# Kernel tuning notes

Measured on AMD Instinct MI355X. Metric: run time of the kernel, lower is better.

Reference implementation:

```python
import jax, jax.numpy as jnp
import numpy as np

IN_DIM = 256
QK_DIM = IN_DIM // 8


def setup_inputs() -> dict:
    key = jax.random.key(0)
    ks = jax.random.split(key, 6)
    x = jax.random.normal(ks[0], (8, IN_DIM, 64, 64), dtype=jnp.float32)
    # 1x1 conv == per-pixel linear; store weights as [out, in]
    q_w = jax.random.normal(ks[1], (QK_DIM, IN_DIM), dtype=jnp.float32) * (1.0 / np.sqrt(IN_DIM))
    q_b = jax.random.normal(ks[2], (QK_DIM,), dtype=jnp.float32) * 0.01
    v_w = jax.random.normal(ks[3], (IN_DIM, IN_DIM), dtype=jnp.float32) * (1.0 / np.sqrt(IN_DIM))
    v_b = jax.random.normal(ks[4], (IN_DIM,), dtype=jnp.float32) * 0.01
    gamma = jnp.zeros((1,), dtype=jnp.float32) + 0.5  # nonzero so attention branch contributes
    return {"x": x, "q_w": q_w, "q_b": q_b, "v_w": v_w, "v_b": v_b, "gamma": gamma}


def reference(x, q_w, q_b, v_w, v_b, gamma):
    b, c, h, w = x.shape
    n = h * w
    xf = x.reshape(b, c, n)                                    # [b, c, n]
    # NOTE: original forward uses q_conv for BOTH q and k (k_conv unused)
    q = jnp.einsum('oc,bcn->bon', q_w, xf) + q_b[None, :, None]  # [b, d, n]
    proj_q = jnp.transpose(q, (0, 2, 1))                       # [b, n, d]
    energy = jnp.einsum('bid,bdj->bij', proj_q, q)             # [b, n, n]
    attention = jax.nn.softmax(energy, axis=-1)
    v = jnp.einsum('oc,bcn->bon', v_w, xf) + v_b[None, :, None]  # [b, c, n]
    # out[b,c,i] = sum_j v[b,c,j] * attention[b,i,j]
    out = jnp.einsum('bcj,bij->bci', v, attention)
    out = out.reshape(b, c, h, w)
    return gamma * out + x
```

## Files before the change

### kernel.cpp

```cpp
#include <hip/hip_runtime.h>

#define B_   8
#define C_   256
#define D_   32
#define N_   4096
#define FMX  64.0f
#define PSWZ(u) ((u) ^ (((u) >> 3) & 7))
#define VP   4112
#define VBUF 32896

typedef __attribute__((ext_vector_type(8))) short bf8_t;
typedef __attribute__((ext_vector_type(4))) float f4_t;

__device__ __forceinline__ unsigned short f2bf(float f) {
    unsigned int u = __builtin_bit_cast(unsigned int, f);
    u += 0x7FFFu + ((u >> 16) & 1u);
    return (unsigned short)(u >> 16);
}
__device__ __forceinline__ float bf2f(unsigned short h) {
    unsigned int u = ((unsigned int)h) << 16;
    return __builtin_bit_cast(float, u);
}
__device__ __forceinline__ uint4 pack8(const unsigned short* h) {
    uint4 u;
    u.x = h[0] | ((unsigned)h[1] << 16); u.y = h[2] | ((unsigned)h[3] << 16);
    u.z = h[4] | ((unsigned)h[5] << 16); u.w = h[6] | ((unsigned)h[7] << 16);
    return u;
}
__device__ __forceinline__ void gload_lds16(const void* g, void* l) {
    __builtin_amdgcn_global_load_lds(
        (const __attribute__((address_space(1))) unsigned int*)g,
        (__attribute__((address_space(3))) unsigned int*)l, 16, 0, 0);
}

__global__ __launch_bounds__(256) void wprep_kernel(
    const float* __restrict__ qw, const float* __restrict__ vw,
    unsigned short* __restrict__ wqFh, unsigned short* __restrict__ wqFl,
    unsigned short* __restrict__ wvF)
{
    const int tid = blockIdx.x * 256 + threadIdx.x;
    if (tid < 8192) {
        const int k = tid;
        const int rowblk = k >> 9, kk = (k >> 6) & 7, lane = k & 63;
        const int oc = rowblk * 16 + (lane & 15), c0 = kk * 32 + (lane >> 4) * 8;
        const float* src = vw + oc * 256 + c0;
        unsigned short h[8];
        #pragma unroll
        for (int e = 0; e < 8; ++e) h[e] = f2bf(src[e]);
        *(uint4*)(wvF + (size_t)k * 8) = pack8(h);
    } else if (tid < 9216) {
        const int k = tid - 8192;
        const int rowblk = k >> 9, kk = (k >> 6) & 7, lane = k & 63;
        const int oc = rowblk * 16 + (lane & 15), c0 = kk * 32 + (lane >> 4) * 8;
        const float* src = qw + oc * 256 + c0;
        unsigned short h[8], l[8];
        #pragma unroll
        for (int e = 0; e < 8; ++e) {
            h[e] = f2bf(src[e]);
            l[e] = f2bf(src[e] - bf2f(h[e]));
        }
        *(uint4*)(wqFh + (size_t)k * 8) = pack8(h);
        *(uint4*)(wqFl + (size_t)k * 8) = pack8(l);
    }
}

__global__ __launch_bounds__(256, 2) void proj_kernel(
    const float* __restrict__ x, const unsigned short* __restrict__ wqFh,
    const unsigned short* __restrict__ wqFl, const unsigned short* __restrict__ wvF,
    const float* __restrict__ qb, const float* __restrict__ vb,
    unsigned short* __restrict__ qh, unsigned short* __restrict__ ql,
    unsigned short* __restrict__ vF)
{
    __shared__ __align__(16) unsigned short S[18432];

    const int t    = threadIdx.x;
    const int lane = t & 63;
    const int w    = t >> 6;
    const int q4   = lane >> 4;
    const int l15  = lane & 15;
    const int b    = blockIdx.x & 7;
    const int tile = blockIdx.x >> 3;
    const int i0   = tile * 64;

    const float* xb = x + (size_t)b * C_ * N_ + i0 + lane;
    #pragma unroll
    for (int cc = 0; cc < 8; ++cc) {
        const int chi = w * 8 + cc;
        float v[8];
        #pragma unroll
        for (int e = 0; e < 8; ++e) v[e] = xb[(size_t)(chi * 8 + e) * N_];
        unsigned short h[8];
        #pragma unroll
        for (int e = 0; e < 8; ++e) h[e] = f2bf(v[e]);
        *(uint4*)&S[(chi * 64 + lane) * 8] = pack8(h);
    }
    __syncthreads();

    f4_t acc[4][4];
    #pragma unroll
    for (int mt = 0; mt < 4; ++mt)
        #pragma unroll
        for (int nt = 0; nt < 4; ++nt) acc[mt][nt] = (f4_t)0.0f;
    f4_t qacc[2];
    qacc[0] = (f4_t)0.0f; qacc[1] = (f4_t)0.0f;

    #pragma unroll
    for (int kk = 0; kk < 8; ++kk) {
        bf8_t Bh[4];
        #pragma unroll
        for (int nt = 0; nt < 4; ++nt)
            Bh[nt] = *(const bf8_t*)&S[((kk * 4 + q4) * 64 + nt * 16 + l15) * 8];
        bf8_t Av[4];
        #pragma unroll
        for (int mt = 0; mt < 4; ++mt)
            Av[mt] = *(const bf8_t*)&wvF[(size_t)(((w * 4 + mt) * 8 + kk) * 64 + lane) * 8];
        bf8_t Aqh[2], Aql[2];
        #pragma unroll
        for (int mq = 0; mq < 2; ++mq) {
            Aqh[mq] = *(const bf8_t*)&wqFh[(size_t)((mq * 8 + kk) * 64 + lane) * 8];
            Aql[mq] = *(const bf8_t*)&wqFl[(size_t)((mq * 8 + kk) * 64 + lane) * 8];
        }

        #pragma unroll
        for (int mt = 0; mt < 4; ++mt)
            #pragma unroll
            for (int nt = 0; nt < 4; ++nt)
                acc[mt][nt] = __builtin_amdgcn_mfma_f32_16x16x32_bf16(
                    Av[mt], Bh[nt], acc[mt][nt], 0, 0, 0);
        #pragma unroll
        for (int mq = 0; mq < 2; ++mq) {
            qacc[mq] = __builtin_amdgcn_mfma_f32_16x16x32_bf16(Aqh[mq], Bh[w], qacc[mq], 0, 0, 0);
            qacc[mq] = __builtin_amdgcn_mfma_f32_16x16x32_bf16(Aql[mq], Bh[w], qacc[mq], 0, 0, 0);
        }
    }

    {
        const int iq = i0 + w * 16 + l15;
        #pragma unroll
        for (int mq = 0; mq < 2; ++mq) {
            float4 qb4 = *(const float4*)(qb + mq * 16 + q4 * 4);
            float qv[4] = {qacc[mq][0] + qb4.x, qacc[mq][1] + qb4.y,
                           qacc[mq][2] + qb4.z, qacc[mq][3] + qb4.w};
            unsigned short hr[4], lr[4];
            #pragma unroll
            for (int r = 0; r < 4; ++r) {
                hr[r] = f2bf(qv[r]);
                lr[r] = f2bf(qv[r] - bf2f(hr[r]));
            }
            uint2 uh, ul;
            uh.x = hr[0] | ((unsigned)hr[1] << 16); uh.y = hr[2] | ((unsigned)hr[3] << 16);
            ul.x = lr[0] | ((unsigned)lr[1] << 16); ul.y = lr[2] | ((unsigned)lr[3] << 16);
            size_t qoff = ((size_t)b * N_ + iq) * D_ + mq * 16 + q4 * 4;
            *(uint2*)(qh + qoff) = uh;
            *(uint2*)(ql + qoff) = ul;
        }
    }

    __syncthreads();
    #pragma unroll
    for (int mt = 0; mt < 4; ++mt) {
        float4 vb4 = *(const float4*)(vb + w * 64 + mt * 16 + q4 * 4);
        float bias[4] = {vb4.x, vb4.y, vb4.z, vb4.w};
        #pragma unroll
        for (int nt = 0; nt < 4; ++nt)
            #pragma unroll
            for (int r = 0; r < 4; ++r)
                S[(w * 64 + mt * 16 + q4 * 4 + r) * 72 + nt * 16 + l15] =
                    f2bf(acc[mt][nt][r] + bias[r]);
    }
    __syncthreads();
    #pragma unroll
    for (int k2 = 0; k2 < 8; ++k2) {
        uint4 dat = *(const uint4*)&S[t * 72 + k2 * 8];
        *(uint4*)(vF + ((((size_t)b * 64 + tile) * 8 + k2) * 256 + t) * 8) = dat;
    }
}

__global__ __launch_bounds__(256, 2) void attn_kernel(
    const unsigned short* __restrict__ qh, const unsigned short* __restrict__ ql,
    const unsigned short* __restrict__ vF, const float* __restrict__ x,
    const float* __restrict__ gamma_p, float* __restrict__ out)
{
    __shared__ __align__(16) unsigned char SMEM[2 * VBUF];
    __shared__ __align__(16) unsigned short Pb[4096];
    __shared__ __align__(16) float rowl[64];
    float* T = (float*)SMEM;

    const int t    = threadIdx.x;
    const int lane = t & 63;
    const int w    = t >> 6;
    const int q4   = lane >> 4;
    const int l15  = lane & 15;
    const int b    = blockIdx.x & 7;
    const int i0   = (blockIdx.x >> 3) * 64;

    const unsigned short* qhb = qh + (size_t)b * N_ * D_;
    const unsigned short* qlb = ql + (size_t)b * N_ * D_;
    const unsigned short* vFb = vF + (size_t)b * 1048576;

    bf8_t Ah[4], Al[4];
    #pragma unroll
    for (int mt = 0; mt < 4; ++mt) {
        size_t off = (size_t)(i0 + mt * 16 + l15) * D_ + q4 * 8;
        Ah[mt] = *(const bf8_t*)(qhb + off);
        Al[mt] = *(const bf8_t*)(qlb + off);
    }

    auto STAGE = [&](int jt, int buf) {
        const unsigned short* vj = vFb + (size_t)jt * 16384;
        #pragma unroll
        for (int i = 0; i < 8; ++i) {
            const int c = i * 4 + w;
            const int p = c >> 2, sub = c & 3;
            gload_lds16(vj + c * 512 + lane * 8,
                        &SMEM[buf * VBUF + p * VP + sub * 1024]);
        }
    };

    f4_t acc[4][4];
    #pragma unroll
    for (int mt = 0; mt < 4; ++mt)
        #pragma unroll
        for (int nt = 0; nt < 4; ++nt) acc[mt][nt] = (f4_t)0.0f;

    f4_t lacc[4];
    #pragma unroll
    for (int mt = 0; mt < 4; ++mt) lacc[mt] = (f4_t)0.0f;
    bf8_t onesb;
    #pragma unroll
    for (int e = 0; e < 8; ++e) onesb[e] = (short)0x3F80;

    const int jl = w * 16 + l15;
    const int pprt = jl >> 3, jlo = jl & 7;

    size_t koff0 = (size_t)(0 + w * 16 + l15) * D_ + q4 * 8;
    bf8_t Bh = *(const bf8_t*)(qhb + koff0);
    bf8_t Bl = *(const bf8_t*)(qlb + koff0);
    STAGE(0, 0);

    for (int jt = 0; jt < N_ / 64; ++jt) {
        const int cur = jt & 1;

        f4_t s[4];
        #pragma unroll
        for (int mt = 0; mt < 4; ++mt) {
            f4_t a = (f4_t)0.0f;
            a = __builtin_amdgcn_mfma_f32_16x16x32_bf16(Ah[mt], Bh, a, 0, 0, 0);
            a = __builtin_amdgcn_mfma_f32_16x16x32_bf16(Ah[mt], Bl, a, 0, 0, 0);
            a = __builtin_amdgcn_mfma_f32_16x16x32_bf16(Al[mt], Bh, a, 0, 0, 0);
            s[mt] = a;
        }

        unsigned short pu[4][4];
        #pragma unroll
        for (int mt = 0; mt < 4; ++mt)
            #pragma unroll
            for (int r = 0; r < 4; ++r)
                pu[mt][r] = f2bf(__expf(s[mt][r] - FMX));

        __syncthreads();

        #pragma unroll
        for (int mt = 0; mt < 4; ++mt)
            #pragma unroll
            for (int r = 0; r < 4; ++r) {
                int u = pprt * 64 + mt * 16 + q4 * 4 + r;
                Pb[PSWZ(u) * 8 + jlo] = pu[mt][r];
            }

        __syncthreads();

        const int jn = (jt + 1 < N_ / 64) ? jt + 1 : jt;
        size_t koffn = (size_t)(jn * 64 + w * 16 + l15) * D_ + q4 * 8;
        bf8_t Bh_n = *(const bf8_t*)(qhb + koffn);
        bf8_t Bl_n = *(const bf8_t*)(qlb + koffn);
        if (jt + 1 < N_ / 64) STAGE(jt + 1, cur ^ 1);

        #pragma unroll
        for (int kk = 0; kk < 2; ++kk) {
            bf8_t Af[4], Bf[4];
            #pragma unroll
            for (int nt = 0; nt < 4; ++nt)
                Bf[nt] = *(const bf8_t*)&SMEM[cur * VBUF + (kk * 4 + q4) * VP +
                                              (w * 64 + nt * 16 + l15) * 16];
            #pragma unroll
            for (int mt = 0; mt < 4; ++mt) {
                int u = (kk * 4 + q4) * 64 + mt * 16 + l15;
                Af[mt] = *(const bf8_t*)&Pb[PSWZ(u) * 8];
            }
            #pragma unroll
            for (int mt = 0; mt < 4; ++mt)
                #pragma unroll
                for (int nt = 0; nt < 4; ++nt)
                    acc[mt][nt] = __builtin_amdgcn_mfma_f32_16x16x32_bf16(
                        Af[mt], Bf[nt], acc[mt][nt], 0, 0, 0);
            if (w == 3) {
                #pragma unroll
                for (int mt = 0; mt < 4; ++mt)
                    lacc[mt] = __builtin_amdgcn_mfma_f32_16x16x32_bf16(
                        Af[mt], onesb, lacc[mt], 0, 0, 0);
            }
        }

        Bh = Bh_n; Bl = Bl_n;
    }

    __syncthreads();
    if (w == 3 && l15 == 0) {
        #pragma unroll
        for (int mt = 0; mt < 4; ++mt)
            #pragma unroll
            for (int r = 0; r < 4; ++r)
                rowl[mt * 16 + q4 * 4 + r] = lacc[mt][r];
    }
    __syncthreads();

    const float g = gamma_p[0];
    for (int mt = 0; mt < 4; ++mt) {
        float4 rl = *(float4*)(&rowl[mt * 16 + q4 * 4]);
        float inv[4] = { g / rl.x, g / rl.y, g / rl.z, g / rl.w };
        #pragma unroll
        for (int nt = 0; nt < 4; ++nt)
            #pragma unroll
            for (int r = 0; r < 4; ++r)
                T[(w * 64 + nt * 16 + l15) * 17 + q4 * 4 + r] = acc[mt][nt][r] * inv[r];
        __syncthreads();
        #pragma unroll
        for (int pass = 0; pass < 4; ++pass) {
            int c  = pass * 64 + (t >> 2);
            int ii = (t & 3) * 4;
            float4 o;
            o.x = T[c * 17 + ii];     o.y = T[c * 17 + ii + 1];
            o.z = T[c * 17 + ii + 2]; o.w = T[c * 17 + ii + 3];
            size_t goff = ((size_t)b * C_ + c) * N_ + i0 + mt * 16 + ii;
            float4 xv = *(const float4*)(x + goff);
            o.x += xv.x; o.y += xv.y; o.z += xv.z; o.w += xv.w;
            *(float4*)(out + goff) = o;
        }
        __syncthreads();
    }
}

extern "C" void kernel_launch(void* const* d_in, const int* in_sizes, int n_in,
                              void* d_out, int out_size, void* d_ws, size_t ws_size,
                              hipStream_t stream)
{
    const float* x     = (const float*)d_in[0];
    const float* q_w   = (const float*)d_in[1];
    const float* q_b   = (const float*)d_in[2];
    const float* v_w   = (const float*)d_in[3];
    const float* v_b   = (const float*)d_in[4];
    const float* gamma = (const float*)d_in[5];
    float* out = (float*)d_out;

    unsigned short* ws16 = (unsigned short*)d_ws;
    unsigned short* qhp  = ws16;
    unsigned short* qlp  = ws16 + 1048576;
    unsigned short* vFp  = ws16 + 2097152;
    unsigned short* wvF  = ws16 + 10485760;
    unsigned short* wqFh = wvF + 65536;
    unsigned short* wqFl = wqFh + 8192;

    wprep_kernel<<<36, 256, 0, stream>>>(q_w, v_w, wqFh, wqFl, wvF);
    proj_kernel<<<B_ * (N_ / 64), 256, 0, stream>>>(x, wqFh, wqFl, wvF, q_b, v_b,
                                                    qhp, qlp, vFp);
    attn_kernel<<<B_ * (N_ / 64), 256, 0, stream>>>(qhp, qlp, vFp, x, gamma, out);
}
```

Measured before the change: 227.9 us.

## Shrink projection tiles, XOR-swizzle V layout, double-buffer P, and raise MFMA priority

The projection kernel now processes 32-pixel tiles with half the LDS, twice as many blocks and a higher occupancy bound. Its q projection is limited to two waves, and V is written in an XOR-swizzled layout. The attention kernel drops the padded V stride in favour of that swizzle and double-buffers the P tile, which removes one barrier per iteration. It also sets a higher wave priority around the MFMA loop. The aim is better proj occupancy, fewer bank conflicts and fewer syncs, at the cost of more smaller proj blocks and a more complex, coupled layout.

Result: no change. 225.9 us (-0.9%).

```diff
diff --git a/kernel.cpp b/kernel.cpp
--- a/kernel.cpp
+++ b/kernel.cpp
@@ -6,8 +6,7 @@
 #define N_   4096
 #define FMX  64.0f
 #define PSWZ(u) ((u) ^ (((u) >> 3) & 7))
-#define VP   4112
-#define VBUF 32896
+#define VBUF 32768
 
 typedef __attribute__((ext_vector_type(8))) short bf8_t;
 typedef __attribute__((ext_vector_type(4))) float f4_t;
@@ -64,14 +63,14 @@
     }
 }
 
-__global__ __launch_bounds__(256, 2) void proj_kernel(
+__global__ __launch_bounds__(256, 4) void proj_kernel(
     const float* __restrict__ x, const unsigned short* __restrict__ wqFh,
     const unsigned short* __restrict__ wqFl, const unsigned short* __restrict__ wvF,
     const float* __restrict__ qb, const float* __restrict__ vb,
     unsigned short* __restrict__ qh, unsigned short* __restrict__ ql,
     unsigned short* __restrict__ vF)
 {
-    __shared__ __align__(16) unsigned short S[18432];
+    __shared__ __align__(16) unsigned short S[10240];
 
     const int t    = threadIdx.x;
     const int lane = t & 63;
@@ -79,62 +78,65 @@
     const int q4   = lane >> 4;
     const int l15  = lane & 15;
     const int b    = blockIdx.x & 7;
-    const int tile = blockIdx.x >> 3;
-    const int i0   = tile * 64;
-
-    const float* xb = x + (size_t)b * C_ * N_ + i0 + lane;
-    #pragma unroll
-    for (int cc = 0; cc < 8; ++cc) {
-        const int chi = w * 8 + cc;
-        float v[8];
-        #pragma unroll
-        for (int e = 0; e < 8; ++e) v[e] = xb[(size_t)(chi * 8 + e) * N_];
-        unsigned short h[8];
-        #pragma unroll
-        for (int e = 0; e < 8; ++e) h[e] = f2bf(v[e]);
-        *(uint4*)&S[(chi * 64 + lane) * 8] = pack8(h);
-    }
-    __syncthreads();
-
-    f4_t acc[4][4];
+    const int tt   = blockIdx.x >> 3;
+    const int i0   = tt * 32;
+
+    {
+        const int n  = lane & 31;
+        const int hi = lane >> 5;
+        const float* xb = x + (size_t)b * C_ * N_ + i0 + n;
+        #pragma unroll
+        for (int cc = 0; cc < 4; ++cc) {
+            const int chi = w * 8 + cc * 2 + hi;
+            float v[8];
+            #pragma unroll
+            for (int e = 0; e < 8; ++e) v[e] = xb[(size_t)(chi * 8 + e) * N_];
+            unsigned short h[8];
+            #pragma unroll
+            for (int e = 0; e < 8; ++e) h[e] = f2bf(v[e]);
+            *(uint4*)&S[(chi * 32 + (n ^ (chi & 3))) * 8] = pack8(h);
+        }
+    }
+    __syncthreads();
+
+    f4_t acc[4][2];
     #pragma unroll
     for (int mt = 0; mt < 4; ++mt)
         #pragma unroll
-        for (int nt = 0; nt < 4; ++nt) acc[mt][nt] = (f4_t)0.0f;
+        for (int nt = 0; nt < 2; ++nt) acc[mt][nt] = (f4_t)0.0f;
     f4_t qacc[2];
     qacc[0] = (f4_t)0.0f; qacc[1] = (f4_t)0.0f;
 
     #pragma unroll
     for (int kk = 0; kk < 8; ++kk) {
-        bf8_t Bh[4];
-        #pragma unroll
-        for (int nt = 0; nt < 4; ++nt)
-            Bh[nt] = *(const bf8_t*)&S[((kk * 4 + q4) * 64 + nt * 16 + l15) * 8];
+        bf8_t Bh[2];
+        #pragma unroll
+        for (int nt = 0; nt < 2; ++nt)
+            Bh[nt] = *(const bf8_t*)&S[((kk * 4 + q4) * 32 + nt * 16 + (l15 ^ q4)) * 8];
         bf8_t Av[4];
         #pragma unroll
         for (int mt = 0; mt < 4; ++mt)
             Av[mt] = *(const bf8_t*)&wvF[(size_t)(((w * 4 + mt) * 8 + kk) * 64 + lane) * 8];
-        bf8_t Aqh[2], Aql[2];
-        #pragma unroll
-        for (int mq = 0; mq < 2; ++mq) {
-            Aqh[mq] = *(const bf8_t*)&wqFh[(size_t)((mq * 8 + kk) * 64 + lane) * 8];
-            Aql[mq] = *(const bf8_t*)&wqFl[(size_t)((mq * 8 + kk) * 64 + lane) * 8];
-        }
-
-        #pragma unroll
-        for (int mt = 0; mt < 4; ++mt)
-            #pragma unroll
-            for (int nt = 0; nt < 4; ++nt)
+
+        #pragma unroll
+        for (int mt = 0; mt < 4; ++mt)
+            #pragma unroll
+            for (int nt = 0; nt < 2; ++nt)
                 acc[mt][nt] = __builtin_amdgcn_mfma_f32_16x16x32_bf16(
                     Av[mt], Bh[nt], acc[mt][nt], 0, 0, 0);
-        #pragma unroll
-        for (int mq = 0; mq < 2; ++mq) {
-            qacc[mq] = __builtin_amdgcn_mfma_f32_16x16x32_bf16(Aqh[mq], Bh[w], qacc[mq], 0, 0, 0);
-            qacc[mq] = __builtin_amdgcn_mfma_f32_16x16x32_bf16(Aql[mq], Bh[w], qacc[mq], 0, 0, 0);
-        }
-    }
-
-    {
+
+        if (w < 2) {
+            #pragma unroll
+            for (int mq = 0; mq < 2; ++mq) {
+                bf8_t Aqh = *(const bf8_t*)&wqFh[(size_t)((mq * 8 + kk) * 64 + lane) * 8];
+                bf8_t Aql = *(const bf8_t*)&wqFl[(size_t)((mq * 8 + kk) * 64 + lane) * 8];
+                qacc[mq] = __builtin_amdgcn_mfma_f32_16x16x32_bf16(Aqh, Bh[w], qacc[mq], 0, 0, 0);
+                qacc[mq] = __builtin_amdgcn_mfma_f32_16x16x32_bf16(Aql, Bh[w], qacc[mq], 0, 0, 0);
+            }
+        }
+    }
+
+    if (w < 2) {
         const int iq = i0 + w * 16 + l15;
         #pragma unroll
         for (int mq = 0; mq < 2; ++mq) {
@@ -162,17 +164,21 @@
         float4 vb4 = *(const float4*)(vb + w * 64 + mt * 16 + q4 * 4);
         float bias[4] = {vb4.x, vb4.y, vb4.z, vb4.w};
         #pragma unroll
-        for (int nt = 0; nt < 4; ++nt)
+        for (int nt = 0; nt < 2; ++nt)
             #pragma unroll
             for (int r = 0; r < 4; ++r)
-                S[(w * 64 + mt * 16 + q4 * 4 + r) * 72 + nt * 16 + l15] =
+                S[(w * 64 + mt * 16 + q4 * 4 + r) * 40 + nt * 16 + l15] =
                     f2bf(acc[mt][nt][r] + bias[r]);
     }
     __syncthreads();
     #pragma unroll
-    for (int k2 = 0; k2 < 8; ++k2) {
-        uint4 dat = *(const uint4*)&S[t * 72 + k2 * 8];
-        *(uint4*)(vF + ((((size_t)b * 64 + tile) * 8 + k2) * 256 + t) * 8) = dat;
+    for (int k2 = 0; k2 < 4; ++k2) {
+        int id  = k2 * 256 + t;
+        int oc  = id >> 2, seg = id & 3;
+        uint4 dat = *(const uint4*)&S[oc * 40 + seg * 8];
+        size_t p  = (size_t)(tt & 1) * 4 + seg;
+        size_t off = ((((size_t)b * 64 + (tt >> 1)) * 8 + p) * 256 + (oc ^ seg)) * 8;
+        *(uint4*)(vF + off) = dat;
     }
 }
 
@@ -182,9 +188,9 @@
     const float* __restrict__ gamma_p, float* __restrict__ out)
 {
     __shared__ __align__(16) unsigned char SMEM[2 * VBUF];
-    __shared__ __align__(16) unsigned short Pb[4096];
-    __shared__ __align__(16) float rowl[64];
-    float* T = (float*)SMEM;
+    __shared__ __align__(16) unsigned short Pb[2][4096];
+    float* T    = (float*)SMEM;
+    float* rowl = (float*)&Pb[0][0];
 
     const int t    = threadIdx.x;
     const int lane = t & 63;
@@ -211,9 +217,7 @@
         #pragma unroll
         for (int i = 0; i < 8; ++i) {
             const int c = i * 4 + w;
-            const int p = c >> 2, sub = c & 3;
-            gload_lds16(vj + c * 512 + lane * 8,
-                        &SMEM[buf * VBUF + p * VP + sub * 1024]);
+            gload_lds16(vj + c * 512 + lane * 8, &SMEM[buf * VBUF + c * 1024]);
         }
     };
 
@@ -233,7 +237,7 @@
     const int jl = w * 16 + l15;
     const int pprt = jl >> 3, jlo = jl & 7;
 
-    size_t koff0 = (size_t)(0 + w * 16 + l15) * D_ + q4 * 8;
+    size_t koff0 = (size_t)(w * 16 + l15) * D_ + q4 * 8;
     bf8_t Bh = *(const bf8_t*)(qhb + koff0);
     bf8_t Bl = *(const bf8_t*)(qlb + koff0);
     STAGE(0, 0);
@@ -258,14 +262,12 @@
             for (int r = 0; r < 4; ++r)
                 pu[mt][r] = f2bf(__expf(s[mt][r] - FMX));
 
-        __syncthreads();
-
         #pragma unroll
         for (int mt = 0; mt < 4; ++mt)
             #pragma unroll
             for (int r = 0; r < 4; ++r) {
                 int u = pprt * 64 + mt * 16 + q4 * 4 + r;
-                Pb[PSWZ(u) * 8 + jlo] = pu[mt][r];
+                Pb[cur][PSWZ(u) * 8 + jlo] = pu[mt][r];
             }
 
         __syncthreads();
@@ -276,17 +278,18 @@
         bf8_t Bl_n = *(const bf8_t*)(qlb + koffn);
         if (jt + 1 < N_ / 64) STAGE(jt + 1, cur ^ 1);
 
+        __builtin_amdgcn_s_setprio(1);
         #pragma unroll
         for (int kk = 0; kk < 2; ++kk) {
             bf8_t Af[4], Bf[4];
             #pragma unroll
             for (int nt = 0; nt < 4; ++nt)
-                Bf[nt] = *(const bf8_t*)&SMEM[cur * VBUF + (kk * 4 + q4) * VP +
-                                              (w * 64 + nt * 16 + l15) * 16];
+                Bf[nt] = *(const bf8_t*)&SMEM[cur * VBUF + (kk * 4 + q4) * 4096 +
+                                              ((w * 64 + nt * 16 + l15) ^ q4) * 16];
             #pragma unroll
             for (int mt = 0; mt < 4; ++mt) {
                 int u = (kk * 4 + q4) * 64 + mt * 16 + l15;
-                Af[mt] = *(const bf8_t*)&Pb[PSWZ(u) * 8];
+                Af[mt] = *(const bf8_t*)&Pb[cur][PSWZ(u) * 8];
             }
             #pragma unroll
             for (int mt = 0; mt < 4; ++mt)
@@ -301,6 +304,7 @@
                         Af[mt], onesb, lacc[mt], 0, 0, 0);
             }
         }
+        __builtin_amdgcn_s_setprio(0);
 
         Bh = Bh_n; Bl = Bl_n;
     }
@@ -362,7 +366,7 @@
     unsigned short* wqFl = wqFh + 8192;
 
     wprep_kernel<<<36, 256, 0, stream>>>(q_w, v_w, wqFh, wqFl, wvF);
-    proj_kernel<<<B_ * (N_ / 64), 256, 0, stream>>>(x, wqFh, wqFl, wvF, q_b, v_b,
+    proj_kernel<<<B_ * (N_ / 32), 256, 0, stream>>>(x, wqFh, wqFl, wvF, q_b, v_b,
                                                     qhp, qlp, vFp);
     attn_kernel<<<B_ * (N_ / 64), 256, 0, stream>>>(qhp, qlp, vFp, x, gamma, out);
 }
```
